# Kernel optimization log

Measured on AMD Instinct MI355X. Metric: run time of the kernel, lower is better.

## Reference

```python
import jax, jax.numpy as jnp
import numpy as np

N_Q = 10000
B, S = 128, 200
M = 50          # memory_size
DK = 64         # memory_key_state_dim == q_embed_dim == final_fc_dim
DV = 128        # memory_value_state_dim == qa_embed_dim
F = 64          # final_fc_dim


def setup_inputs() -> dict:
    key = jax.random.key(0)
    ks = jax.random.split(key, 14)
    q_data = jax.random.randint(ks[0], (B, S), 0, N_Q + 1)
    qa_data = jax.random.randint(ks[1], (B, S), 0, 2 * N_Q + 1)
    # target in {-1 (pad), 0, 1}
    target = jax.random.randint(ks[2], (B, S), -1, 2).astype(jnp.float32)
    q_embed_w = jax.random.normal(ks[3], (N_Q + 1, DK), jnp.float32) * 0.1
    q_embed_w = q_embed_w.at[0].set(0.0)  # padding_idx=0
    qa_embed_w = jax.random.normal(ks[4], (2 * N_Q + 1, DV), jnp.float32) * 0.1
    qa_embed_w = qa_embed_w.at[0].set(0.0)
    mem_key = jax.random.normal(ks[5], (M, DK), jnp.float32) * (2.0 / DK) ** 0.5
    init_mem_value = jax.random.normal(ks[6], (M, DV), jnp.float32) * (2.0 / DV) ** 0.5
    erase_w = jax.random.normal(ks[7], (DV, DV), jnp.float32) * (2.0 / DV) ** 0.5
    erase_b = jnp.zeros((DV,), jnp.float32)
    add_w = jax.random.normal(ks[8], (DV, DV), jnp.float32) * (2.0 / DV) ** 0.5
    add_b = jnp.zeros((DV,), jnp.float32)
    read_w = jax.random.normal(ks[9], (F, DV + F), jnp.float32) * (2.0 / (DV + F)) ** 0.5
    read_b = jnp.zeros((F,), jnp.float32)
    pred_w = jax.random.normal(ks[10], (1, F), jnp.float32) * (2.0 / F) ** 0.5
    pred_b = jnp.zeros((1,), jnp.float32)
    return {
        'q_data': q_data, 'qa_data': qa_data, 'target': target,
        'q_embed_w': q_embed_w, 'qa_embed_w': qa_embed_w,
        'mem_key': mem_key, 'init_mem_value': init_mem_value,
        'erase_w': erase_w, 'erase_b': erase_b,
        'add_w': add_w, 'add_b': add_b,
        'read_w': read_w, 'read_b': read_b,
        'pred_w': pred_w, 'pred_b': pred_b,
    }


def reference(q_data, qa_data, target, q_embed_w, qa_embed_w, mem_key,
              init_mem_value, erase_w, erase_b, add_w, add_b,
              read_w, read_b, pred_w, pred_b):
    q_e = q_embed_w[q_data]    # [B,S,DK]
    qa_e = qa_embed_w[qa_data]  # [B,S,DV]
    Mv0 = jnp.broadcast_to(init_mem_value, (q_data.shape[0],) + init_mem_value.shape)  # [B,M,DV]

    def step(Mv, x):
        q, qa = x                                           # [B,DK], [B,DV]
        w = jax.nn.softmax(q @ mem_key.T, axis=1)           # addressing -> [B,M]
        read = jnp.einsum('bm,bmv->bv', w, Mv)              # weighted read (before write)
        e = jax.nn.sigmoid(qa @ erase_w.T + erase_b)        # [B,DV]
        a = jnp.tanh(qa @ add_w.T + add_b)                  # [B,DV]
        Mv_new = Mv * (1.0 - w[:, :, None] * e[:, None, :]) + w[:, :, None] * a[:, None, :]
        return Mv_new, read

    _, reads = jax.lax.scan(step, Mv0, (q_e.transpose(1, 0, 2), qa_e.transpose(1, 0, 2)))
    reads = reads.transpose(1, 0, 2)                        # [B,S,DV]

    h = jnp.tanh(jnp.concatenate([reads, q_e], axis=-1) @ read_w.T + read_b)  # [B,S,F]
    logits = (h @ pred_w.T + pred_b)[..., 0]                # [B,S]

    mask = target >= 0
    t = jnp.where(mask, target, 0.0)
    # stable BCE with logits
    bce = jnp.maximum(logits, 0.0) - logits * t + jnp.log1p(jnp.exp(-jnp.abs(logits)))
    n_valid = jnp.maximum(jnp.sum(mask.astype(jnp.float32)), 1.0)
    loss = jnp.sum(jnp.where(mask, bce, 0.0)) / n_valid
    probs = jnp.where(mask, jax.nn.sigmoid(logits), 0.0)    # masked predictions, fixed shape
    return loss, probs
```

## Files before the change

### kernel.cpp

```cpp
#include <hip/hip_runtime.h>
#include <math.h>

#define BB 128
#define SS 200
#define MM 50
#define DKK 64
#define DVV 128
#define FF 64
#define NROW (BB*SS)

#define WROW 64
#define NFCB (NROW/64)
#define WLDS 136
#define CLEN 25
#define MP 25
#define NSCB 100

#define W_OFF   0L
#define EA_OFF  (W_OFF + (long)NROW*WROW)
#define R_OFF   (EA_OFF + (long)NROW*DVV*2)
#define ACC_OFF (R_OFF + (long)NROW*DVV)

typedef __attribute__((ext_vector_type(8))) short bf16x8;
typedef __attribute__((ext_vector_type(4))) float f32x4;
typedef __attribute__((ext_vector_type(2))) float f32x2;

__device__ __forceinline__ float rlane(float v, int l) {
    return __builtin_bit_cast(float, __builtin_amdgcn_readlane(__builtin_bit_cast(unsigned, v), l));
}
__device__ __forceinline__ short f2bf(float f) {
    unsigned u = __builtin_bit_cast(unsigned, f);
    u += 0x7fff + ((u >> 16) & 1);
    return (short)(u >> 16);
}

__global__ __launch_bounds__(256) void k_pre(const int* __restrict__ q_data,
                                             const float* __restrict__ q_embed_w,
                                             const float* __restrict__ mem_key,
                                             const int* __restrict__ qa_data,
                                             const float* __restrict__ qa_embed_w,
                                             const float* __restrict__ erase_w,
                                             const float* __restrict__ erase_b,
                                             const float* __restrict__ add_w,
                                             const float* __restrict__ add_b,
                                             float* __restrict__ w_out,
                                             float* __restrict__ EA,
                                             float* __restrict__ acc) {
    __shared__ union {
        short  wl[2 * 128 * WLDS];
        float4 mk[MM * 16];
    } sh;
    int tid = threadIdx.x;
    int bid = blockIdx.x;

    if (bid < NSCB) {
        if (bid == 0 && tid == 0) {
            acc[0] = 0.f; acc[1] = 0.f;
            ((unsigned*)acc)[2] = 0u;
        }
        const float4* mkg = (const float4*)mem_key;
        for (int i = tid; i < MM * 16; i += 256) sh.mk[i] = mkg[i];
        __syncthreads();

        int item = bid * 256 + tid;
        int qidx = q_data[item];
        const float4* qg = (const float4*)(q_embed_w + (long)qidx * DKK);
        float4 q[16];
#pragma unroll
        for (int i = 0; i < 16; i++) q[i] = qg[i];

        float s[MM];
        float mx = -1e30f;
#pragma unroll 2
        for (int m = 0; m < MM; m++) {
            float a = 0.f;
#pragma unroll
            for (int k4 = 0; k4 < 16; k4++) {
                float4 mkv = sh.mk[m * 16 + k4];
                float4 qv = q[k4];
                a = fmaf(qv.x, mkv.x, a);
                a = fmaf(qv.y, mkv.y, a);
                a = fmaf(qv.z, mkv.z, a);
                a = fmaf(qv.w, mkv.w, a);
            }
            s[m] = a;
            mx = fmaxf(mx, a);
        }
        float sum = 0.f;
#pragma unroll
        for (int m = 0; m < MM; m++) { s[m] = expf(s[m] - mx); sum += s[m]; }
        float inv = 1.f / sum;

        float* wo = w_out + (long)item * WROW;
#pragma unroll
        for (int m = 0; m < MM; m++) wo[m] = s[m] * inv;
#pragma unroll
        for (int m = MM; m < WROW; m++) wo[m] = 0.f;
        return;
    }

    int r0 = (bid - NSCB) * 64;
    int lane = tid & 63;
    int wv = tid >> 6;
    int n = lane & 15;
    int quad = lane >> 4;

    for (int i = tid; i < 8192; i += 256) {
        int mat = i >> 12;
        int r = (i >> 5) & 127;
        int p = i & 31;
        float4 src = *(const float4*)((mat ? add_w : erase_w) + r * 128 + p * 4);
        short4 d;
        d.x = f2bf(src.x); d.y = f2bf(src.y); d.z = f2bf(src.z); d.w = f2bf(src.w);
        *(short4*)(sh.wl + (mat * 128 + r) * WLDS + p * 4) = d;
    }

    int arow = r0 + wv * 16 + n;
    int qidx = qa_data[arow];
    const float* qp = qa_embed_w + (long)qidx * DVV + quad * 8;
    bf16x8 afrag[4];
#pragma unroll
    for (int kb = 0; kb < 4; kb++) {
        float4 lo = *(const float4*)(qp + kb * 32);
        float4 hi = *(const float4*)(qp + kb * 32 + 4);
        bf16x8 f;
        f[0] = f2bf(lo.x); f[1] = f2bf(lo.y); f[2] = f2bf(lo.z); f[3] = f2bf(lo.w);
        f[4] = f2bf(hi.x); f[5] = f2bf(hi.y); f[6] = f2bf(hi.z); f[7] = f2bf(hi.w);
        afrag[kb] = f;
    }

    float eb_[8], ab_[8];
#pragma unroll
    for (int vt = 0; vt < 8; vt++) {
        eb_[vt] = erase_b[vt * 16 + n];
        ab_[vt] = add_b[vt * 16 + n];
    }
    __syncthreads();

    int rowbase = r0 + wv * 16 + quad * 4;
#pragma unroll 2
    for (int vt = 0; vt < 8; vt++) {
        int vrow = vt * 16 + n;
        f32x4 ae = {0.f, 0.f, 0.f, 0.f};
        f32x4 aa = {0.f, 0.f, 0.f, 0.f};
#pragma unroll
        for (int kb = 0; kb < 4; kb++) {
            bf16x8 be = *(const bf16x8*)(sh.wl + vrow * WLDS + kb * 32 + quad * 8);
            bf16x8 ba = *(const bf16x8*)(sh.wl + (128 + vrow) * WLDS + kb * 32 + quad * 8);
            ae = __builtin_amdgcn_mfma_f32_16x16x32_bf16(afrag[kb], be, ae, 0, 0, 0);
            aa = __builtin_amdgcn_mfma_f32_16x16x32_bf16(afrag[kb], ba, aa, 0, 0, 0);
        }
        int v = vt * 16 + n;
        float eb = eb_[vt], ab = ab_[vt];
#pragma unroll
        for (int r = 0; r < 4; r++) {
            float ev = 1.f / (1.f + __expf(-(ae[r] + eb)));
            float av = 2.f / (1.f + __expf(-2.f * (aa[r] + ab))) - 1.f;
            float2 o; o.x = ev; o.y = av;
            *(float2*)(EA + (((long)(rowbase + r)) * DVV + v) * 2) = o;
        }
    }
}

__global__ __launch_bounds__(512, 2) void k_scan(const float* __restrict__ w_pad,
                                                 const float* __restrict__ EA,
                                                 const float* __restrict__ init_mv,
                                                 float* __restrict__ R) {
    __shared__ float Sb[MM * 64];
    int b   = blockIdx.x >> 1;
    int vh  = blockIdx.x & 1;
    int tid = threadIdx.x;
    int lane  = tid & 63;
    int chunk = tid >> 6;
    int v  = vh * 64 + lane;
    int t0 = chunk * CLEN;

    const float* wbase = w_pad + ((long)b * SS + t0) * WROW;
    const float* eab   = EA + (((long)b * SS + t0) * DVV + v) * 2;
    float*       Rb    = R + ((long)b * SS + t0) * DVV + v;

    const f32x2 one = {1.f, 1.f};

    f32x2 A2[MP], B2[MP];
#pragma unroll
    for (int j = 0; j < MP; j++) { A2[j] = one; B2[j] = (f32x2){0.f, 0.f}; }

    float  w_cur  = wbase[lane];
    float2 ea_cur = *(const float2*)eab;
#pragma unroll 1
    for (int t = 0; t < CLEN; t++) {
        int tp = (t + 1 < CLEN) ? t + 1 : t;
        float  w_nxt  = wbase[tp * WROW + lane];
        float2 ea_nxt = *(const float2*)(eab + (long)tp * DVV * 2);
        f32x2 e2 = {ea_cur.x, ea_cur.x};
        f32x2 a2 = {ea_cur.y, ea_cur.y};
#pragma unroll
        for (int j = 0; j < MP; j++) {
            f32x2 w2 = {rlane(w_cur, 2 * j), rlane(w_cur, 2 * j + 1)};
            f32x2 alpha = one - w2 * e2;
            A2[j] = A2[j] * alpha;
            B2[j] = alpha * B2[j] + w2 * a2;
        }
        w_cur = w_nxt; ea_cur = ea_nxt;
    }

    f32x2 Mv[MP];
    if (chunk == 0) {
#pragma unroll
        for (int j = 0; j < MP; j++) {
            Mv[j].x = init_mv[(2 * j) * DVV + v];
            Mv[j].y = init_mv[(2 * j + 1) * DVV + v];
        }
#pragma unroll
        for (int j = 0; j < MP; j++) {
            f32x2 nb = A2[j] * Mv[j] + B2[j];
            Sb[(2 * j) * 64 + lane] = nb.x;
            Sb[(2 * j + 1) * 64 + lane] = nb.y;
        }
    }
    __syncthreads();
    for (int c = 1; c < 8; c++) {
        if (chunk == c) {
#pragma unroll
            for (int j = 0; j < MP; j++) {
                Mv[j].x = Sb[(2 * j) * 64 + lane];
                Mv[j].y = Sb[(2 * j + 1) * 64 + lane];
            }
            if (c < 7) {
#pragma unroll
                for (int j = 0; j < MP; j++) {
                    f32x2 nb = A2[j] * Mv[j] + B2[j];
                    Sb[(2 * j) * 64 + lane] = nb.x;
                    Sb[(2 * j + 1) * 64 + lane] = nb.y;
                }
            }
        }
        __syncthreads();
    }

    w_cur  = wbase[lane];
    ea_cur = *(const float2*)eab;
#pragma unroll 1
    for (int t = 0; t < CLEN; t++) {
        int tp = (t + 1 < CLEN) ? t + 1 : t;
        float  w_nxt  = wbase[tp * WROW + lane];
        float2 ea_nxt = *(const float2*)(eab + (long)tp * DVV * 2);
        f32x2 e2 = {ea_cur.x, ea_cur.x};
        f32x2 a2 = {ea_cur.y, ea_cur.y};
        f32x2 rd2 = {0.f, 0.f};
#pragma unroll
        for (int j = 0; j < MP; j++) {
            f32x2 w2 = {rlane(w_cur, 2 * j), rlane(w_cur, 2 * j + 1)};
            rd2 = rd2 + w2 * Mv[j];
            f32x2 alpha = one - w2 * e2;
            Mv[j] = alpha * Mv[j] + w2 * a2;
        }
        Rb[t * DVV] = rd2.x + rd2.y;
        w_cur = w_nxt; ea_cur = ea_nxt;
    }
}

__global__ __launch_bounds__(256) void k_fc(const float* __restrict__ Rr,
                                            const int* __restrict__ q_data,
                                            const float* __restrict__ q_embed_w,
                                            const float* __restrict__ read_w,
                                            const float* __restrict__ read_b,
                                            const float* __restrict__ pred_w,
                                            const float* __restrict__ pred_b,
                                            const float* __restrict__ target,
                                            float* __restrict__ out,
                                            float* __restrict__ acc) {
    __shared__ float Wl[64 * 196];
    __shared__ float xl[64 * 100];
    __shared__ float2 red[4];
    int tid = threadIdx.x;
    int r0 = blockIdx.x * 64;
    int fq = tid & 15;
    int rh = tid >> 4;

    for (int i = tid; i < 3072; i += 256) {
        int f = i / 48, p = i - f * 48;
        *(float4*)(Wl + f * 196 + p * 4) = *(const float4*)(read_w + f * 192 + p * 4);
    }

    float accv[4][4];
#pragma unroll
    for (int i = 0; i < 4; i++)
#pragma unroll
        for (int j = 0; j < 4; j++) accv[i][j] = 0.f;

    for (int kc = 0; kc < 2; kc++) {
        __syncthreads();
        for (int i = tid; i < 1536; i += 256) {
            int r = i / 24, p = i - r * 24;
            float4 val;
            if (kc == 0) {
                val = *(const float4*)(Rr + (long)(r0 + r) * DVV + p * 4);
            } else if (p < 8) {
                val = *(const float4*)(Rr + (long)(r0 + r) * DVV + 96 + p * 4);
            } else {
                int qi = q_data[r0 + r];
                val = *(const float4*)(q_embed_w + (long)qi * DKK + (p - 8) * 4);
            }
            *(float4*)(xl + r * 100 + p * 4) = val;
        }
        __syncthreads();
#pragma unroll 4
        for (int kk = 0; kk < 96; kk += 4) {
            float4 wv[4], x4[4];
#pragma unroll
            for (int i = 0; i < 4; i++)
                wv[i] = *(const float4*)(Wl + (fq + 16 * i) * 196 + kc * 96 + kk);
#pragma unroll
            for (int j = 0; j < 4; j++)
                x4[j] = *(const float4*)(xl + (rh * 4 + j) * 100 + kk);
#pragma unroll
            for (int i = 0; i < 4; i++)
#pragma unroll
                for (int j = 0; j < 4; j++) {
                    accv[i][j] = fmaf(x4[j].x, wv[i].x, accv[i][j]);
                    accv[i][j] = fmaf(x4[j].y, wv[i].y, accv[i][j]);
                    accv[i][j] = fmaf(x4[j].z, wv[i].z, accv[i][j]);
                    accv[i][j] = fmaf(x4[j].w, wv[i].w, accv[i][j]);
                }
        }
    }

    float pb = pred_b[0];
    float rb_[4], pw_[4];
#pragma unroll
    for (int i = 0; i < 4; i++) { rb_[i] = read_b[fq + 16 * i]; pw_[i] = pred_w[fq + 16 * i]; }

    float bce_sum = 0.f, cnt = 0.f;
#pragma unroll
    for (int j = 0; j < 4; j++) {
        float pv = 0.f;
#pragma unroll
        for (int i = 0; i < 4; i++)
            pv = fmaf(pw_[i], tanhf(accv[i][j] + rb_[i]), pv);
        pv += __shfl_xor(pv, 1, 64);
        pv += __shfl_xor(pv, 2, 64);
        pv += __shfl_xor(pv, 4, 64);
        pv += __shfl_xor(pv, 8, 64);
        if (fq == 0) {
            int row = r0 + rh * 4 + j;
            float tgt = target[row];
            float logit = pv + pb;
            float prob = 0.f;
            if (tgt >= 0.f) {
                prob = 1.f / (1.f + expf(-logit));
                float bce = fmaxf(logit, 0.f) - logit * tgt + log1pf(expf(-fabsf(logit)));
                bce_sum += bce;
                cnt += 1.f;
            }
            out[1 + row] = prob;
        }
    }
    bce_sum += __shfl_xor(bce_sum, 16, 64);
    bce_sum += __shfl_xor(bce_sum, 32, 64);
    cnt     += __shfl_xor(cnt, 16, 64);
    cnt     += __shfl_xor(cnt, 32, 64);
    int lane = tid & 63, wid = tid >> 6;
    if (lane == 0) { red[wid].x = bce_sum; red[wid].y = cnt; }
    __syncthreads();
    if (tid == 0) {
        float bsum = red[0].x + red[1].x + red[2].x + red[3].x;
        float csum = red[0].y + red[1].y + red[2].y + red[3].y;
        atomicAdd(&acc[0], bsum);
        atomicAdd(&acc[1], csum);
        __threadfence();
        unsigned prev = atomicAdd((unsigned*)acc + 2, 1u);
        if (prev == NFCB - 1) {
            __threadfence();
            float B = atomicAdd(&acc[0], 0.f);
            float C = atomicAdd(&acc[1], 0.f);
            out[0] = B / fmaxf(C, 1.f);
        }
    }
}

extern "C" void kernel_launch(void* const* d_in, const int* in_sizes, int n_in,
                              void* d_out, int out_size, void* d_ws, size_t ws_size,
                              hipStream_t stream) {
    const int*   q_data     = (const int*)d_in[0];
    const int*   qa_data    = (const int*)d_in[1];
    const float* target     = (const float*)d_in[2];
    const float* q_embed_w  = (const float*)d_in[3];
    const float* qa_embed_w = (const float*)d_in[4];
    const float* mem_key    = (const float*)d_in[5];
    const float* init_mv    = (const float*)d_in[6];
    const float* erase_w    = (const float*)d_in[7];
    const float* erase_b    = (const float*)d_in[8];
    const float* add_w      = (const float*)d_in[9];
    const float* add_b      = (const float*)d_in[10];
    const float* read_w     = (const float*)d_in[11];
    const float* read_b     = (const float*)d_in[12];
    const float* pred_w     = (const float*)d_in[13];
    const float* pred_b     = (const float*)d_in[14];
    float* out = (float*)d_out;
    float* ws  = (float*)d_ws;

    float* w_all = ws + W_OFF;
    float* EA    = ws + EA_OFF;
    float* R     = ws + R_OFF;
    float* acc   = ws + ACC_OFF;

    k_pre<<<NSCB + NROW / 64, 256, 0, stream>>>(q_data, q_embed_w, mem_key,
                                                qa_data, qa_embed_w,
                                                erase_w, erase_b, add_w, add_b,
                                                w_all, EA, acc);
    k_scan<<<BB * 2, 512, 0, stream>>>(w_all, EA, init_mv, R);
    k_fc<<<NFCB, 256, 0, stream>>>(R, q_data, q_embed_w, read_w, read_b,
                                   pred_w, pred_b, target, out, acc);
}
```

Measured before the change: 194.3 us.

## Use bf16 MFMA for the read/predict FC layer in k_fc

Replaces the scalar FP32 FMA GEMM in the final FC kernel with bf16 16x16x32 MFMA instructions. The read_w tile is converted to bf16 in LDS, and the reads/q-embedding operands are loaded straight into register fragments, which removes the x staging buffer and a barrier. tanh and exp are replaced with fast __expf-based forms. This cuts ALU and LDS work in the FC stage at the cost of bf16 rounding of the activations and weights, which may shift the logits slightly. The FC kernel is likely a small share of total time compared with the sequential scan.

```diff
diff --git a/kernel.cpp b/kernel.cpp
--- a/kernel.cpp
+++ b/kernel.cpp
@@ -12,6 +12,7 @@
 #define WROW 64
 #define NFCB (NROW/64)
 #define WLDS 136
+#define FLDS 200
 #define CLEN 25
 #define MP 25
 #define NSCB 100
@@ -32,6 +33,14 @@
     unsigned u = __builtin_bit_cast(unsigned, f);
     u += 0x7fff + ((u >> 16) & 1);
     return (short)(u >> 16);
+}
+__device__ __forceinline__ bf16x8 cvt8(const float* p) {
+    float4 lo = *(const float4*)p;
+    float4 hi = *(const float4*)(p + 4);
+    bf16x8 f;
+    f[0] = f2bf(lo.x); f[1] = f2bf(lo.y); f[2] = f2bf(lo.z); f[3] = f2bf(lo.w);
+    f[4] = f2bf(hi.x); f[5] = f2bf(hi.y); f[6] = f2bf(hi.z); f[7] = f2bf(hi.w);
+    return f;
 }
 
 __global__ __launch_bounds__(256) void k_pre(const int* __restrict__ q_data,
@@ -120,14 +129,7 @@
     const float* qp = qa_embed_w + (long)qidx * DVV + quad * 8;
     bf16x8 afrag[4];
 #pragma unroll
-    for (int kb = 0; kb < 4; kb++) {
-        float4 lo = *(const float4*)(qp + kb * 32);
-        float4 hi = *(const float4*)(qp + kb * 32 + 4);
-        bf16x8 f;
-        f[0] = f2bf(lo.x); f[1] = f2bf(lo.y); f[2] = f2bf(lo.z); f[3] = f2bf(lo.w);
-        f[4] = f2bf(hi.x); f[5] = f2bf(hi.y); f[6] = f2bf(hi.z); f[7] = f2bf(hi.w);
-        afrag[kb] = f;
-    }
+    for (int kb = 0; kb < 4; kb++) afrag[kb] = cvt8(qp + kb * 32);
 
     float eb_[8], ab_[8];
 #pragma unroll
@@ -270,86 +272,77 @@
                                             const float* __restrict__ target,
                                             float* __restrict__ out,
                                             float* __restrict__ acc) {
-    __shared__ float Wl[64 * 196];
-    __shared__ float xl[64 * 100];
+    __shared__ short Wl[64 * FLDS];
     __shared__ float2 red[4];
     int tid = threadIdx.x;
     int r0 = blockIdx.x * 64;
-    int fq = tid & 15;
-    int rh = tid >> 4;
+    int lane = tid & 63;
+    int wv = tid >> 6;
+    int n = lane & 15;
+    int quad = lane >> 4;
 
     for (int i = tid; i < 3072; i += 256) {
         int f = i / 48, p = i - f * 48;
-        *(float4*)(Wl + f * 196 + p * 4) = *(const float4*)(read_w + f * 192 + p * 4);
-    }
-
-    float accv[4][4];
-#pragma unroll
-    for (int i = 0; i < 4; i++)
-#pragma unroll
-        for (int j = 0; j < 4; j++) accv[i][j] = 0.f;
-
-    for (int kc = 0; kc < 2; kc++) {
-        __syncthreads();
-        for (int i = tid; i < 1536; i += 256) {
-            int r = i / 24, p = i - r * 24;
-            float4 val;
-            if (kc == 0) {
-                val = *(const float4*)(Rr + (long)(r0 + r) * DVV + p * 4);
-            } else if (p < 8) {
-                val = *(const float4*)(Rr + (long)(r0 + r) * DVV + 96 + p * 4);
-            } else {
-                int qi = q_data[r0 + r];
-                val = *(const float4*)(q_embed_w + (long)qi * DKK + (p - 8) * 4);
-            }
-            *(float4*)(xl + r * 100 + p * 4) = val;
-        }
-        __syncthreads();
-#pragma unroll 4
-        for (int kk = 0; kk < 96; kk += 4) {
-            float4 wv[4], x4[4];
-#pragma unroll
-            for (int i = 0; i < 4; i++)
-                wv[i] = *(const float4*)(Wl + (fq + 16 * i) * 196 + kc * 96 + kk);
-#pragma unroll
-            for (int j = 0; j < 4; j++)
-                x4[j] = *(const float4*)(xl + (rh * 4 + j) * 100 + kk);
-#pragma unroll
-            for (int i = 0; i < 4; i++)
-#pragma unroll
-                for (int j = 0; j < 4; j++) {
-                    accv[i][j] = fmaf(x4[j].x, wv[i].x, accv[i][j]);
-                    accv[i][j] = fmaf(x4[j].y, wv[i].y, accv[i][j]);
-                    accv[i][j] = fmaf(x4[j].z, wv[i].z, accv[i][j]);
-                    accv[i][j] = fmaf(x4[j].w, wv[i].w, accv[i][j]);
-                }
-        }
-    }
-
+        float4 src = *(const float4*)(read_w + f * 192 + p * 4);
+        short4 d;
+        d.x = f2bf(src.x); d.y = f2bf(src.y); d.z = f2bf(src.z); d.w = f2bf(src.w);
+        *(short4*)(Wl + f * FLDS + p * 4) = d;
+    }
+
+    int arow = r0 + wv * 16 + n;
+    const float* rp = Rr + (long)arow * DVV + quad * 8;
+    int qi = q_data[arow];
+    const float* qp = q_embed_w + (long)qi * DKK + quad * 8;
+    bf16x8 afrag[6];
+#pragma unroll
+    for (int kb = 0; kb < 4; kb++) afrag[kb] = cvt8(rp + kb * 32);
+#pragma unroll
+    for (int kb = 0; kb < 2; kb++) afrag[4 + kb] = cvt8(qp + kb * 32);
+
+    float rb_[4], pw_[4];
+#pragma unroll
+    for (int ft = 0; ft < 4; ft++) {
+        rb_[ft] = read_b[ft * 16 + n];
+        pw_[ft] = pred_w[ft * 16 + n];
+    }
     float pb = pred_b[0];
-    float rb_[4], pw_[4];
-#pragma unroll
-    for (int i = 0; i < 4; i++) { rb_[i] = read_b[fq + 16 * i]; pw_[i] = pred_w[fq + 16 * i]; }
+    __syncthreads();
+
+    int rowbase = r0 + wv * 16 + quad * 4;
+    float pv[4] = {0.f, 0.f, 0.f, 0.f};
+#pragma unroll
+    for (int ft = 0; ft < 4; ft++) {
+        int f = ft * 16 + n;
+        f32x4 ac = {0.f, 0.f, 0.f, 0.f};
+#pragma unroll
+        for (int kb = 0; kb < 6; kb++) {
+            bf16x8 bfr = *(const bf16x8*)(Wl + f * FLDS + kb * 32 + quad * 8);
+            ac = __builtin_amdgcn_mfma_f32_16x16x32_bf16(afrag[kb], bfr, ac, 0, 0, 0);
+        }
+        float rb = rb_[ft], pw = pw_[ft];
+#pragma unroll
+        for (int r = 0; r < 4; r++) {
+            float h = 2.f / (1.f + __expf(-2.f * (ac[r] + rb))) - 1.f;
+            pv[r] = fmaf(pw, h, pv[r]);
+        }
+    }
 
     float bce_sum = 0.f, cnt = 0.f;
 #pragma unroll
-    for (int j = 0; j < 4; j++) {
-        float pv = 0.f;
-#pragma unroll
-        for (int i = 0; i < 4; i++)
-            pv = fmaf(pw_[i], tanhf(accv[i][j] + rb_[i]), pv);
-        pv += __shfl_xor(pv, 1, 64);
-        pv += __shfl_xor(pv, 2, 64);
-        pv += __shfl_xor(pv, 4, 64);
-        pv += __shfl_xor(pv, 8, 64);
-        if (fq == 0) {
-            int row = r0 + rh * 4 + j;
+    for (int r = 0; r < 4; r++) {
+        float p = pv[r];
+        p += __shfl_xor(p, 1, 64);
+        p += __shfl_xor(p, 2, 64);
+        p += __shfl_xor(p, 4, 64);
+        p += __shfl_xor(p, 8, 64);
+        if (n == 0) {
+            int row = rowbase + r;
             float tgt = target[row];
-            float logit = pv + pb;
+            float logit = p + pb;
             float prob = 0.f;
             if (tgt >= 0.f) {
-                prob = 1.f / (1.f + expf(-logit));
-                float bce = fmaxf(logit, 0.f) - logit * tgt + log1pf(expf(-fabsf(logit)));
+                prob = 1.f / (1.f + __expf(-logit));
+                float bce = fmaxf(logit, 0.f) - logit * tgt + log1pf(__expf(-fabsf(logit)));
                 bce_sum += bce;
                 cnt += 1.f;
             }
@@ -360,8 +353,7 @@
     bce_sum += __shfl_xor(bce_sum, 32, 64);
     cnt     += __shfl_xor(cnt, 16, 64);
     cnt     += __shfl_xor(cnt, 32, 64);
-    int lane = tid & 63, wid = tid >> 6;
-    if (lane == 0) { red[wid].x = bce_sum; red[wid].y = cnt; }
+    if (lane == 0) { red[wv].x = bce_sum; red[wv].y = cnt; }
     __syncthreads();
     if (tid == 0) {
         float bsum = red[0].x + red[1].x + red[2].x + red[3].x;
```

Measured after the change: 182.5 us. 1.06x faster.
